# Performance work log

Measured on AMD Instinct MI355X. Metric: run time of the kernel, lower is better.

The kernel has to match this reference:

```python
import jax, jax.numpy as jnp
import numpy as np

B, T, D, H = 32, 2048, 512, 512


def setup_inputs() -> dict:
    key = jax.random.key(0)
    ks = jax.random.split(key, 6)
    s_in = 1.0 / np.sqrt(D)
    s_hh = 1.0 / np.sqrt(2 * H)
    return {
        "X": jax.random.normal(ks[0], (B, T, D), dtype=jnp.float32),
        "W_p": jax.random.normal(ks[1], (D, H), dtype=jnp.float32) * s_in,
        "b_p": jnp.zeros((H,), dtype=jnp.float32),
        "W_f": jax.random.normal(ks[2], (2 * H, H), dtype=jnp.float32) * s_hh,
        "b_f": jnp.zeros((H,), dtype=jnp.float32),
        "W_i": jax.random.normal(ks[3], (2 * H, H), dtype=jnp.float32) * s_hh,
        "b_i": jnp.zeros((H,), dtype=jnp.float32),
        "W_c": jax.random.normal(ks[4], (2 * H, H), dtype=jnp.float32) * s_hh,
        "b_c": jnp.zeros((H,), dtype=jnp.float32),
        "W_o": jax.random.normal(ks[5], (2 * H, H), dtype=jnp.float32) * s_hh,
        "b_o": jnp.zeros((H,), dtype=jnp.float32),
    }


def reference(X, W_p, b_p, W_f, b_f, W_i, b_i, W_c, b_c, W_o, b_o):
    batch, hidden = X.shape[0], W_p.shape[1]
    # Precompute the input projection for all timesteps (parallel over T).
    proj = jnp.tanh(jnp.einsum("btd,dh->bth", X, W_p) + b_p)  # [B,T,H]

    def step(carry, p_t):
        h, c = carry
        g = jnp.concatenate([p_t, h], axis=1)  # [B, 2H]
        f = jax.nn.sigmoid(g @ W_f + b_f)
        i = jax.nn.sigmoid(g @ W_i + b_i)
        cg = jnp.tanh(g @ W_c + b_c)
        o = jax.nn.sigmoid(g @ W_o + b_o)
        c_new = f * c + i * cg
        h_new = o * jnp.tanh(c_new)
        return (h_new, c_new), h_new

    init = (jnp.zeros((batch, hidden), X.dtype), jnp.zeros((batch, hidden), X.dtype))
    _, states = jax.lax.scan(step, init, jnp.swapaxes(proj, 0, 1))  # states: [T,B,H]
    return jnp.swapaxes(states, 0, 1)  # [B,T,H]
```

## Files before the change

### kernel.cpp

```cpp
#include <hip/hip_runtime.h>
#include <stdint.h>

#define BB 32
#define TT 2048
#define DD 512
#define HH 512
#define NG 2048

typedef short bf16x8 __attribute__((ext_vector_type(8)));
typedef float f32x4  __attribute__((ext_vector_type(4)));
typedef float f32x16 __attribute__((ext_vector_type(16)));
typedef unsigned long long u64;

__device__ __forceinline__ unsigned short f2bf(float f) {
    union { float f; uint32_t u; } v; v.f = f;
    uint32_t u = v.u;
    return (unsigned short)((u + 0x7fffu + ((u >> 16) & 1u)) >> 16);
}
__device__ __forceinline__ float fast_tanh(float x) {
    float ax = fabsf(x);
    float e = __expf(2.0f * ax);
    float t = 1.0f - 2.0f / (e + 1.0f);
    return copysignf(t, x);
}
__device__ __forceinline__ float fast_sig(float x) {
    return 1.0f / (1.0f + __expf(-x));
}

__global__ void k_convert_x(const float* __restrict__ X, unsigned short* __restrict__ Xb) {
    int i = (blockIdx.x * 256 + threadIdx.x) * 4;
    float4 v = *(const float4*)(X + i);
    ushort4 o;
    o.x = f2bf(v.x); o.y = f2bf(v.y); o.z = f2bf(v.z); o.w = f2bf(v.w);
    *(ushort4*)(Xb + i) = o;
}

__global__ void k_prep_wp(const float* __restrict__ Wp, unsigned short* __restrict__ WpT) {
    int idx = blockIdx.x * 256 + threadIdx.x;
    int n = idx >> 9, k = idx & 511;
    WpT[idx] = f2bf(Wp[k * HH + n]);
}

__global__ void k_prep_u(const float* __restrict__ Wf, const float* __restrict__ Wi,
                         const float* __restrict__ Wc, const float* __restrict__ Wo,
                         const float* __restrict__ bf_, const float* __restrict__ bi_,
                         const float* __restrict__ bc_, const float* __restrict__ bo_,
                         unsigned short* __restrict__ WtopT, unsigned short* __restrict__ UT,
                         float* __restrict__ biascat) {
    int idx = blockIdx.x * 256 + threadIdx.x;
    int col = idx >> 9, k = idx & 511;
    int g = col & 3, hid = col >> 2;
    const float* W = (g == 0) ? Wf : (g == 1) ? Wi : (g == 2) ? Wc : Wo;
    WtopT[idx] = f2bf(W[k * HH + hid]);
    UT[idx]    = f2bf(W[(HH + k) * HH + hid]);
    if (k == 0) {
        const float* bp = (g == 0) ? bf_ : (g == 1) ? bi_ : (g == 2) ? bc_ : bo_;
        biascat[col] = bp[hid];
    }
}

__global__ void k_zero(unsigned short* __restrict__ hbuf, int* __restrict__ flags) {
    int i = blockIdx.x * 256 + threadIdx.x;
    hbuf[i] = 0;
    if (i < 64) flags[i] = 0;
}

__global__ __launch_bounds__(256)
void k_gemm_a1(const unsigned short* __restrict__ A, const unsigned short* __restrict__ BT,
               const float* __restrict__ bias, unsigned short* __restrict__ projF,
               int M, int N, int K) {
    __shared__ unsigned short lA[128 * 32];
    __shared__ unsigned short lB[128 * 32];
    const int tid  = threadIdx.x;
    const int wave = tid >> 6, lane = tid & 63;
    const int q = lane >> 4, ln = lane & 15;
    const int tm = blockIdx.x * 128, tn = blockIdx.y * 128;
    const int mtb = (wave >> 1) * 64, ntb = (wave & 1) * 64;
    f32x4 acc[4][4] = {};

    for (int kc = 0; kc < K; kc += 32) {
        __syncthreads();
        #pragma unroll
        for (int r = 0; r < 2; ++r) {
            int row = r * 64 + wave * 16 + (lane >> 2);
            const unsigned short* ga = A  + (size_t)(tm + row) * K + kc + (lane & 3) * 8;
            const unsigned short* gb = BT + (size_t)(tn + row) * K + kc + (lane & 3) * 8;
            __builtin_amdgcn_global_load_lds(
                (const __attribute__((address_space(1))) uint32_t*)ga,
                (__attribute__((address_space(3))) uint32_t*)&lA[(r * 64 + wave * 16) * 32],
                16, 0, 0);
            __builtin_amdgcn_global_load_lds(
                (const __attribute__((address_space(1))) uint32_t*)gb,
                (__attribute__((address_space(3))) uint32_t*)&lB[(r * 64 + wave * 16) * 32],
                16, 0, 0);
        }
        __syncthreads();
        bf16x8 af[4], bfr[4];
        #pragma unroll
        for (int i = 0; i < 4; ++i) {
            af[i]  = *(const bf16x8*)&lA[(mtb + i * 16 + ln) * 32 + q * 8];
            bfr[i] = *(const bf16x8*)&lB[(ntb + i * 16 + ln) * 32 + q * 8];
        }
        #pragma unroll
        for (int mi = 0; mi < 4; ++mi)
            #pragma unroll
            for (int ni = 0; ni < 4; ++ni)
                acc[mi][ni] = __builtin_amdgcn_mfma_f32_16x16x32_bf16(af[mi], bfr[ni], acc[mi][ni], 0, 0, 0);
    }

    #pragma unroll
    for (int ni = 0; ni < 4; ++ni) {
        int col = tn + ntb + ni * 16 + ln;
        float bz = bias[col];
        int hb2 = (col >> 5) * 1024 + ((col >> 4) & 1) * 512
                + ((col >> 3) & 1) * 256 + (col & 7);
        #pragma unroll
        for (int mi = 0; mi < 4; ++mi) {
            #pragma unroll
            for (int r = 0; r < 4; ++r) {
                int row = tm + mtb + mi * 16 + q * 4 + r;
                int b = row >> 11, t = row & (TT - 1);
                float v = acc[mi][ni][r] + bz;
                projF[(size_t)t * 16384 + hb2 + b * 8] = f2bf(fast_tanh(v));
            }
        }
    }
}

__global__ __launch_bounds__(512) __attribute__((amdgpu_waves_per_eu(2, 2)))
void k_lstm_seq(const unsigned short* __restrict__ projF,
                const unsigned short* __restrict__ WtopT,
                const unsigned short* __restrict__ UT,
                const float* __restrict__ biascat,
                unsigned short* __restrict__ hbuf,
                int* __restrict__ flags,
                float* __restrict__ out) {
    const int nb   = blockIdx.x;
    const int tid  = threadIdx.x;
    const int wv   = tid >> 6;
    const int l    = tid & 63;
    const int ct   = wv >> 1;
    const int kh   = wv & 1;
    const int lcol = l & 31;
    const int hi   = l >> 5;

    __shared__ __align__(16) unsigned short lh[16384];
    __shared__ __align__(16) unsigned short projLds[2][16384];
    __shared__ float preact[2][32][132];

    {
        const unsigned short* ps = projF + (size_t)(wv * 4) * 512 + l * 8;
        #pragma unroll
        for (int f = 0; f < 4; ++f) {
            __builtin_amdgcn_global_load_lds(
                (const __attribute__((address_space(1))) uint32_t*)(ps + f * 512),
                (__attribute__((address_space(3))) uint32_t*)&projLds[0][(wv * 4 + f) * 512],
                16, 0, 0);
        }
    }

    const size_t wbase = (size_t)(nb * 128 + ct * 32 + lcol) * 512;
    bf16x8 wtf[16], uf[16];
    #pragma unroll
    for (int j = 0; j < 16; ++j) {
        int ks = kh * 16 + j;
        wtf[j] = *(const bf16x8*)(WtopT + wbase + ks * 16 + hi * 8);
        uf[j]  = *(const bf16x8*)(UT    + wbase + ks * 16 + hi * 8);
    }
    #pragma unroll
    for (int j = 0; j < 16; ++j) {
        asm volatile("" : "+v"(wtf[j]));
        asm volatile("" : "+v"(uf[j]));
    }

    const int b0  = tid >> 4;
    const int hl0 = (tid * 2) & 31;
    float bias8[8];
    #pragma unroll
    for (int k = 0; k < 8; ++k) bias8[k] = biascat[nb * 128 + hl0 * 4 + k];
    float c0 = 0.f, c1 = 0.f;

    const int ksc = nb * 2 + (hl0 >> 4);
    const int hic = (hl0 >> 3) & 1;
    const int ec  = hl0 & 7;
    uint32_t* const pub0 = (uint32_t*)hbuf + (size_t)ksc * 256 + (hic * 32 + b0) * 4 + (ec >> 1);

    __syncthreads();

    for (int t = 0; t < TT; ++t) {
        const int rb = (t & 1) ^ 1, wb = t & 1;

        f32x16 accA = {}, accB = {};
        {
            const char* pb = (const char*)&projLds[t & 1][0] + (kh * 16) * 1024 + l * 16;
            #pragma unroll
            for (int j = 0; j < 16; j += 2) {
                bf16x8 a0 = *(const bf16x8*)(pb + j * 1024);
                bf16x8 a1 = *(const bf16x8*)(pb + (j + 1) * 1024);
                accA = __builtin_amdgcn_mfma_f32_32x32x16_bf16(a0, wtf[j],     accA, 0, 0, 0);
                accB = __builtin_amdgcn_mfma_f32_32x32x16_bf16(a1, wtf[j + 1], accB, 0, 0, 0);
            }
        }

        if (t + 1 < TT) {
            const unsigned short* ps = projF + (size_t)(t + 1) * 16384 + (size_t)(wv * 4) * 512 + l * 8;
            #pragma unroll
            for (int f = 0; f < 4; ++f) {
                __builtin_amdgcn_global_load_lds(
                    (const __attribute__((address_space(1))) uint32_t*)(ps + f * 512),
                    (__attribute__((address_space(3))) uint32_t*)&projLds[(t + 1) & 1][(wv * 4 + f) * 512],
                    16, 0, 0);
            }
        }

        if (t > 0 && wv == 0) {
            int v;
            do {
                v = __hip_atomic_load(&flags[l & 15], __ATOMIC_RELAXED, __HIP_MEMORY_SCOPE_AGENT);
            } while (!__all(v >= t));
        }
        __syncthreads();

        {
            const u64* hb = (const u64*)hbuf + (size_t)rb * 4096;
            u64 st[8];
            #pragma unroll
            for (int r = 0; r < 8; ++r)
                st[r] = __hip_atomic_load(hb + r * 512 + tid, __ATOMIC_RELAXED, __HIP_MEMORY_SCOPE_AGENT);
            u64* lh64 = (u64*)lh;
            #pragma unroll
            for (int r = 0; r < 8; ++r)
                lh64[r * 512 + tid] = st[r];
        }
        __syncthreads();

        {
            const char* lbase = (const char*)lh + (kh * 16) * 1024 + l * 16;
            #pragma unroll
            for (int j = 0; j < 16; j += 2) {
                bf16x8 a0 = *(const bf16x8*)(lbase + j * 1024);
                bf16x8 a1 = *(const bf16x8*)(lbase + (j + 1) * 1024);
                accA = __builtin_amdgcn_mfma_f32_32x32x16_bf16(a0, uf[j],     accA, 0, 0, 0);
                accB = __builtin_amdgcn_mfma_f32_32x32x16_bf16(a1, uf[j + 1], accB, 0, 0, 0);
            }
        }

        #pragma unroll
        for (int reg = 0; reg < 16; ++reg) {
            int b = (reg & 3) + 8 * (reg >> 2) + 4 * hi;
            preact[kh][b][ct * 32 + lcol] = accA[reg] + accB[reg];
        }
        __syncthreads();

        const float* p0 = &preact[0][b0][hl0 * 4];
        const float* p1 = &preact[1][b0][hl0 * 4];
        float f0 = fast_sig (p0[0] + p1[0] + bias8[0]);
        float i0 = fast_sig (p0[1] + p1[1] + bias8[1]);
        float g0 = fast_tanh(p0[2] + p1[2] + bias8[2]);
        float o0 = fast_sig (p0[3] + p1[3] + bias8[3]);
        c0 = f0 * c0 + i0 * g0;
        float h0 = o0 * fast_tanh(c0);

        float f1 = fast_sig (p0[4] + p1[4] + bias8[4]);
        float i1 = fast_sig (p0[5] + p1[5] + bias8[5]);
        float g1 = fast_tanh(p0[6] + p1[6] + bias8[6]);
        float o1 = fast_sig (p0[7] + p1[7] + bias8[7]);
        c1 = f1 * c1 + i1 * g1;
        float h1 = o1 * fast_tanh(c1);

        uint32_t packed = (uint32_t)f2bf(h0) | ((uint32_t)f2bf(h1) << 16);
        __hip_atomic_store(pub0 + (size_t)wb * 8192, packed,
                           __ATOMIC_RELAXED, __HIP_MEMORY_SCOPE_AGENT);

        __syncthreads();
        if (tid == 0)
            __hip_atomic_store(&flags[nb], t + 1, __ATOMIC_RELAXED, __HIP_MEMORY_SCOPE_AGENT);

        float2 ho; ho.x = h0; ho.y = h1;
        *(float2*)&out[((size_t)b0 * TT + t) * HH + nb * 32 + hl0] = ho;
    }
}

extern "C" void kernel_launch(void* const* d_in, const int* in_sizes, int n_in,
                              void* d_out, int out_size, void* d_ws, size_t ws_size,
                              hipStream_t stream) {
    const float* X   = (const float*)d_in[0];
    const float* Wp  = (const float*)d_in[1];
    const float* bp  = (const float*)d_in[2];
    const float* Wf  = (const float*)d_in[3];
    const float* bf_ = (const float*)d_in[4];
    const float* Wi  = (const float*)d_in[5];
    const float* bi_ = (const float*)d_in[6];
    const float* Wc  = (const float*)d_in[7];
    const float* bc_ = (const float*)d_in[8];
    const float* Wo  = (const float*)d_in[9];
    const float* bo_ = (const float*)d_in[10];
    float* out = (float*)d_out;

    char* w = (char*)d_ws;
    auto alloc = [&](size_t bytes) {
        char* p = w;
        w += (bytes + 255) & ~(size_t)255;
        return p;
    };
    unsigned short* projF  = (unsigned short*)alloc((size_t)BB * TT * HH * 2);
    unsigned short* WpT    = (unsigned short*)alloc((size_t)DD * HH * 2);
    unsigned short* WtopT  = (unsigned short*)alloc((size_t)NG * HH * 2);
    unsigned short* UT     = (unsigned short*)alloc((size_t)NG * HH * 2);
    float*          biascat= (float*)alloc(NG * 4);
    unsigned short* hbuf   = (unsigned short*)alloc(2 * BB * HH * 2);
    int*            flags  = (int*)alloc(1024);

    unsigned short* Xb = (unsigned short*)d_out;

    k_convert_x<<<(BB * TT * DD) / (256 * 4), 256, 0, stream>>>(X, Xb);
    k_prep_wp<<<(DD * HH) / 256, 256, 0, stream>>>(Wp, WpT);
    k_prep_u<<<(NG * HH) / 256, 256, 0, stream>>>(Wf, Wi, Wc, Wo, bf_, bi_, bc_, bo_,
                                                  WtopT, UT, biascat);
    k_zero<<<128, 256, 0, stream>>>(hbuf, flags);

    k_gemm_a1<<<dim3((BB * TT) / 128, HH / 128), 256, 0, stream>>>(Xb, WpT, bp, projF,
                                                                   BB * TT, HH, DD);
    k_lstm_seq<<<16, 512, 0, stream>>>(projF, WtopT, UT, biascat, hbuf, flags, out);
}
```

Before: 6.830 ms.

## Specialize waves: half compute input projection ahead, half do recurrent h matmul

The eight waves are split into two groups. Four waves compute the input-projection matmul for step t+1 while the other four do the recurrent h·U matmul over the full K for step t. Previously every wave did both halves of K serially on the critical path. This aims to take the projection MFMAs off the latency-critical recurrence, at the cost of doubling the K-depth of the recurrent matmul per wave. It also adds a prefetch two steps ahead and a second preact buffer.

Result: no change. 6.956 ms (+1.9%).

```diff
diff --git a/kernel.cpp b/kernel.cpp
--- a/kernel.cpp
+++ b/kernel.cpp
@@ -139,39 +139,37 @@
     const int tid  = threadIdx.x;
     const int wv   = tid >> 6;
     const int l    = tid & 63;
-    const int ct   = wv >> 1;
-    const int kh   = wv & 1;
+    const bool hwave = (wv < 4);
+    const int ct   = wv & 3;
     const int lcol = l & 31;
     const int hi   = l >> 5;
 
     __shared__ __align__(16) unsigned short lh[16384];
     __shared__ __align__(16) unsigned short projLds[2][16384];
-    __shared__ float preact[2][32][132];
+    __shared__ float preact_h[32][132];
+    __shared__ float preact_pj[2][32][132];
 
     {
-        const unsigned short* ps = projF + (size_t)(wv * 4) * 512 + l * 8;
-        #pragma unroll
-        for (int f = 0; f < 4; ++f) {
+        unsigned short* pl = (unsigned short*)projLds;
+        #pragma unroll
+        for (int c = 0; c < 8; ++c) {
+            const unsigned short* ps = projF + (size_t)(wv * 4096 + c * 512) + l * 8;
             __builtin_amdgcn_global_load_lds(
-                (const __attribute__((address_space(1))) uint32_t*)(ps + f * 512),
-                (__attribute__((address_space(3))) uint32_t*)&projLds[0][(wv * 4 + f) * 512],
+                (const __attribute__((address_space(1))) uint32_t*)ps,
+                (__attribute__((address_space(3))) uint32_t*)&pl[wv * 4096 + c * 512],
                 16, 0, 0);
         }
     }
 
+    const unsigned short* Wsrc = hwave ? UT : WtopT;
     const size_t wbase = (size_t)(nb * 128 + ct * 32 + lcol) * 512;
-    bf16x8 wtf[16], uf[16];
+    bf16x8 wfrag[32];
     #pragma unroll
-    for (int j = 0; j < 16; ++j) {
-        int ks = kh * 16 + j;
-        wtf[j] = *(const bf16x8*)(WtopT + wbase + ks * 16 + hi * 8);
-        uf[j]  = *(const bf16x8*)(UT    + wbase + ks * 16 + hi * 8);
-    }
+    for (int j = 0; j < 32; ++j)
+        wfrag[j] = *(const bf16x8*)(Wsrc + wbase + j * 16 + hi * 8);
     #pragma unroll
-    for (int j = 0; j < 16; ++j) {
-        asm volatile("" : "+v"(wtf[j]));
-        asm volatile("" : "+v"(uf[j]));
-    }
+    for (int j = 0; j < 32; ++j)
+        asm volatile("" : "+v"(wfrag[j]));
 
     const int b0  = tid >> 4;
     const int hl0 = (tid * 2) & 31;
@@ -187,37 +185,63 @@
 
     __syncthreads();
 
+    if (!hwave) {
+        f32x16 aA = {}, aB = {};
+        const char* pb = (const char*)&projLds[0][0] + l * 16;
+        #pragma unroll
+        for (int j = 0; j < 32; j += 2) {
+            bf16x8 a0 = *(const bf16x8*)(pb + j * 1024);
+            bf16x8 a1 = *(const bf16x8*)(pb + (j + 1) * 1024);
+            aA = __builtin_amdgcn_mfma_f32_32x32x16_bf16(a0, wfrag[j],     aA, 0, 0, 0);
+            aB = __builtin_amdgcn_mfma_f32_32x32x16_bf16(a1, wfrag[j + 1], aB, 0, 0, 0);
+        }
+        #pragma unroll
+        for (int reg = 0; reg < 16; ++reg) {
+            int b = (reg & 3) + 8 * (reg >> 2) + 4 * hi;
+            preact_pj[0][b][ct * 32 + lcol] = aA[reg] + aB[reg];
+        }
+    }
+    __syncthreads();
+
     for (int t = 0; t < TT; ++t) {
         const int rb = (t & 1) ^ 1, wb = t & 1;
 
-        f32x16 accA = {}, accB = {};
-        {
-            const char* pb = (const char*)&projLds[t & 1][0] + (kh * 16) * 1024 + l * 16;
-            #pragma unroll
-            for (int j = 0; j < 16; j += 2) {
-                bf16x8 a0 = *(const bf16x8*)(pb + j * 1024);
-                bf16x8 a1 = *(const bf16x8*)(pb + (j + 1) * 1024);
-                accA = __builtin_amdgcn_mfma_f32_32x32x16_bf16(a0, wtf[j],     accA, 0, 0, 0);
-                accB = __builtin_amdgcn_mfma_f32_32x32x16_bf16(a1, wtf[j + 1], accB, 0, 0, 0);
-            }
-        }
-
-        if (t + 1 < TT) {
-            const unsigned short* ps = projF + (size_t)(t + 1) * 16384 + (size_t)(wv * 4) * 512 + l * 8;
-            #pragma unroll
-            for (int f = 0; f < 4; ++f) {
-                __builtin_amdgcn_global_load_lds(
-                    (const __attribute__((address_space(1))) uint32_t*)(ps + f * 512),
-                    (__attribute__((address_space(3))) uint32_t*)&projLds[(t + 1) & 1][(wv * 4 + f) * 512],
-                    16, 0, 0);
-            }
-        }
-
-        if (t > 0 && wv == 0) {
-            int v;
-            do {
-                v = __hip_atomic_load(&flags[l & 15], __ATOMIC_RELAXED, __HIP_MEMORY_SCOPE_AGENT);
-            } while (!__all(v >= t));
+        if (hwave) {
+            if (t + 2 < TT) {
+                unsigned short* pl = &projLds[t & 1][0];
+                #pragma unroll
+                for (int c = 0; c < 8; ++c) {
+                    const unsigned short* ps = projF + (size_t)(t + 2) * 16384
+                                             + (size_t)(wv * 4096 + c * 512) + l * 8;
+                    __builtin_amdgcn_global_load_lds(
+                        (const __attribute__((address_space(1))) uint32_t*)ps,
+                        (__attribute__((address_space(3))) uint32_t*)&pl[wv * 4096 + c * 512],
+                        16, 0, 0);
+                }
+            }
+            if (t > 0 && wv == 0) {
+                int v;
+                do {
+                    v = __hip_atomic_load(&flags[l & 15], __ATOMIC_RELAXED, __HIP_MEMORY_SCOPE_AGENT);
+                } while (!__all(v >= t));
+            }
+        } else {
+            if (t + 1 < TT) {
+                f32x16 aA = {}, aB = {};
+                const char* pb = (const char*)&projLds[(t + 1) & 1][0] + l * 16;
+                #pragma unroll
+                for (int j = 0; j < 32; j += 2) {
+                    bf16x8 a0 = *(const bf16x8*)(pb + j * 1024);
+                    bf16x8 a1 = *(const bf16x8*)(pb + (j + 1) * 1024);
+                    aA = __builtin_amdgcn_mfma_f32_32x32x16_bf16(a0, wfrag[j],     aA, 0, 0, 0);
+                    aB = __builtin_amdgcn_mfma_f32_32x32x16_bf16(a1, wfrag[j + 1], aB, 0, 0, 0);
+                }
+                #pragma unroll
+                for (int reg = 0; reg < 16; ++reg) {
+                    int b = (reg & 3) + 8 * (reg >> 2) + 4 * hi;
+                    preact_pj[(t + 1) & 1][b][ct * 32 + lcol] = aA[reg] + aB[reg];
+                }
+            }
         }
         __syncthreads();
 
@@ -234,26 +258,26 @@
         }
         __syncthreads();
 
-        {
-            const char* lbase = (const char*)lh + (kh * 16) * 1024 + l * 16;
-            #pragma unroll
-            for (int j = 0; j < 16; j += 2) {
+        if (hwave) {
+            f32x16 aA = {}, aB = {};
+            const char* lbase = (const char*)lh + l * 16;
+            #pragma unroll
+            for (int j = 0; j < 32; j += 2) {
                 bf16x8 a0 = *(const bf16x8*)(lbase + j * 1024);
                 bf16x8 a1 = *(const bf16x8*)(lbase + (j + 1) * 1024);
-                accA = __builtin_amdgcn_mfma_f32_32x32x16_bf16(a0, uf[j],     accA, 0, 0, 0);
-                accB = __builtin_amdgcn_mfma_f32_32x32x16_bf16(a1, uf[j + 1], accB, 0, 0, 0);
-            }
-        }
-
-        #pragma unroll
-        for (int reg = 0; reg < 16; ++reg) {
-            int b = (reg & 3) + 8 * (reg >> 2) + 4 * hi;
-            preact[kh][b][ct * 32 + lcol] = accA[reg] + accB[reg];
-        }
-        __syncthreads();
-
-        const float* p0 = &preact[0][b0][hl0 * 4];
-        const float* p1 = &preact[1][b0][hl0 * 4];
+                aA = __builtin_amdgcn_mfma_f32_32x32x16_bf16(a0, wfrag[j],     aA, 0, 0, 0);
+                aB = __builtin_amdgcn_mfma_f32_32x32x16_bf16(a1, wfrag[j + 1], aB, 0, 0, 0);
+            }
+            #pragma unroll
+            for (int reg = 0; reg < 16; ++reg) {
+                int b = (reg & 3) + 8 * (reg >> 2) + 4 * hi;
+                preact_h[b][ct * 32 + lcol] = aA[reg] + aB[reg];
+            }
+        }
+        __syncthreads();
+
+        const float* p0 = &preact_h[b0][hl0 * 4];
+        const float* p1 = &preact_pj[t & 1][b0][hl0 * 4];
         float f0 = fast_sig (p0[0] + p1[0] + bias8[0]);
         float i0 = fast_sig (p0[1] + p1[1] + bias8[1]);
         float g0 = fast_tanh(p0[2] + p1[2] + bias8[2]);
```
